# Performance work log

Measured on AMD Instinct MI355X. Metric: run time of the kernel, lower is better.

Reference implementation:

```python
import jax, jax.numpy as jnp
import numpy as np

D_MODEL, D_K, D_V, HEADS = 512, 8, 8, 6
EPS = 1e-5


def setup_inputs() -> dict:
    key = jax.random.key(0)
    ks = jax.random.split(key, 16)
    B, S = 16, 1024
    inp = {
        'q_input': jax.random.normal(ks[0], (B, S, D_MODEL), jnp.float32),
        'k_input': jax.random.normal(ks[1], (B, S, D_MODEL), jnp.float32),
        'v_input': jax.random.normal(ks[2], (B, S, D_MODEL), jnp.float32),
        'mask': jax.random.randint(ks[3], (B, S, S), 0, 2).astype(bool),
        'Wq': jax.random.normal(ks[4], (D_MODEL, D_K * HEADS), jnp.float32) * 0.04,
        'bq': jax.random.normal(ks[5], (D_K * HEADS,), jnp.float32) * 0.02,
        'Wk': jax.random.normal(ks[6], (D_MODEL, D_K * HEADS), jnp.float32) * 0.04,
        'bk': jax.random.normal(ks[7], (D_K * HEADS,), jnp.float32) * 0.02,
        'Wv': jax.random.normal(ks[8], (D_MODEL, D_V * HEADS), jnp.float32) * 0.04,
        'bv': jax.random.normal(ks[9], (D_V * HEADS,), jnp.float32) * 0.02,
        'Wo': jax.random.normal(ks[10], (HEADS * D_K, D_MODEL), jnp.float32) * 0.1,
        'bo': jax.random.normal(ks[11], (D_MODEL,), jnp.float32) * 0.02,
        'ln_w': 1.0 + jax.random.normal(ks[12], (D_MODEL,), jnp.float32) * 0.02,
        'ln_b': jax.random.normal(ks[13], (D_MODEL,), jnp.float32) * 0.02,
    }
    return inp


def reference(q_input, k_input, v_input, mask, Wq, bq, Wk, bk, Wv, bv, Wo, bo, ln_w, ln_b):
    B, S, _ = q_input.shape
    # projections -> [B, H, S, d]
    q_s = (q_input @ Wq + bq).reshape(B, S, HEADS, D_K).transpose(0, 2, 1, 3)
    k_s = (k_input @ Wk + bk).reshape(B, S, HEADS, D_K).transpose(0, 2, 1, 3)
    v_s = (v_input @ Wv + bv).reshape(B, S, HEADS, D_V).transpose(0, 2, 1, 3)
    # scaled dot-product with masked_fill(mask, 1e-9) as in the original (fills VALUE, not -inf)
    scores = jnp.einsum('bhqd,bhkd->bhqk', q_s, k_s) / np.sqrt(D_K).astype(np.float32)
    scores = jnp.where(mask[:, None, :, :], jnp.float32(1e-9), scores)
    attn = jax.nn.softmax(scores, axis=-1)
    out = jnp.einsum('bhqk,bhkd->bhqd', attn, v_s)  # [B,H,S,d_v]
    out = out.transpose(0, 2, 1, 3).reshape(B, S, HEADS * D_K)
    out = out @ Wo + bo
    x = q_input + out  # residual
    mu = jnp.mean(x, axis=-1, keepdims=True)
    var = jnp.var(x, axis=-1, keepdims=True)
    return (x - mu) * jax.lax.rsqrt(var + EPS) * ln_w + ln_b
```

## Files before the change

### kernel.cpp

```cpp
#include <hip/hip_runtime.h>

constexpr int B = 16;
constexpr int S = 1024;
constexpr int DM = 512;
constexpr int H = 6;
constexpr int DK = 8;
constexpr int NJ = H * DK;
constexpr int BS = B * S;
constexpr int WB_ELEMS = 16 * NJ * 32;

typedef __attribute__((ext_vector_type(8))) short bf16x8;
typedef __attribute__((ext_vector_type(8))) _Float16 half8;
typedef __attribute__((ext_vector_type(4))) _Float16 half4;
typedef __attribute__((ext_vector_type(4))) float floatx4;

#define LOG2E 1.4426950408889634f
#define QSCALE (0.35355339059327373f * LOG2E)

__device__ inline ushort f2bf(float f) {
  unsigned int u = __builtin_bit_cast(unsigned int, f);
  return (ushort)((u + 0x7FFFu + ((u >> 16) & 1u)) >> 16);
}

__global__ __launch_bounds__(256) void maskbits_kernel(
    const int* __restrict__ mask, unsigned long long* __restrict__ bits) {
  int wave = threadIdx.x >> 6, lane = threadIdx.x & 63;
  int row = blockIdx.x * 4 + wave;
  const int* mrow = mask + (size_t)row * S;
  unsigned long long* brow = bits + (size_t)row * 16;
  int koff = ((lane >> 5) << 5) + 2 * (lane & 15) + ((lane >> 4) & 1);
#pragma unroll
  for (int c = 0; c < 16; c++) {
    int v = mrow[c * 64 + koff];
    unsigned long long bal = __ballot(v != 0);
    if (lane == 0) brow[c] = bal;
  }
}

__global__ __launch_bounds__(256) void wprep_kernel(
    const float* __restrict__ Wq, const float* __restrict__ Wk,
    const float* __restrict__ Wv, ushort* __restrict__ Wb,
    uint2* __restrict__ VBf) {
  int m = blockIdx.x;
  if (m < 3) {
    const float* W = (m == 0) ? Wq : (m == 1) ? Wk : Wv;
    ushort* dst = Wb + (size_t)m * WB_ELEMS;
    for (int e = threadIdx.x; e < WB_ELEMS; e += 256) {
      int kc = e / 1536;
      int rem = e - kc * 1536;
      int n = rem >> 5, kj = rem & 31;
      dst[e] = f2bf(W[(size_t)(kc * 32 + kj) * NJ + n]);
    }
  } else {
    int bh = m - 3;
    for (int i = threadIdx.x; i < 2048; i += 256) {
      int tile = i >> 5;
      int li = i & 31;
      int g = li >> 3, dd = 8 + (li & 7);
      uint hv = (dd == 8) ? 0x3C003C00u : 0u;
      uint2 val; val.x = hv; val.y = hv;
      VBf[((size_t)bh * 64 + tile) * 64 + g * 16 + dd] = val;
    }
  }
}

__global__ __launch_bounds__(256) void proj_kernel(
    const float* __restrict__ q_in, const float* __restrict__ k_in,
    const float* __restrict__ v_in, const ushort* __restrict__ Wb,
    const float* __restrict__ bq, const float* __restrict__ bk,
    const float* __restrict__ bv,
    ushort* __restrict__ Qo, ushort* __restrict__ Ko, ushort* __restrict__ Vo) {
  int m = blockIdx.y;
  const float* x    = (m == 0) ? q_in : (m == 1) ? k_in : v_in;
  const float* bias = (m == 0) ? bq   : (m == 1) ? bk   : bv;
  ushort* out       = (m == 0) ? Qo   : (m == 1) ? Ko   : Vo;
  float oscale      = (m == 0) ? QSCALE : 1.0f;
  const ushort* Wg  = Wb + (size_t)m * WB_ELEMS;

  __shared__ ushort Wl[WB_ELEMS];

  int t = threadIdx.x;
  {
    const uint4* src = (const uint4*)Wg;
    uint4* dst = (uint4*)Wl;
#pragma unroll
    for (int i = 0; i < 12; i++) dst[t + i * 256] = src[t + i * 256];
  }

  int r0 = blockIdx.x * 64;
  int wave = t >> 6, lane = t & 63;
  int n16 = lane & 15, quad = lane >> 4;
  const float* xrow = x + (size_t)(r0 + wave * 16 + n16) * DM + quad * 8;

  floatx4 acc0 = {0.f, 0.f, 0.f, 0.f};
  floatx4 acc1 = {0.f, 0.f, 0.f, 0.f};
  floatx4 acc2 = {0.f, 0.f, 0.f, 0.f};

  __syncthreads();

#pragma unroll 4
  for (int kc = 0; kc < 16; kc++) {
    float4 xa = *(const float4*)(xrow + kc * 32);
    float4 xb = *(const float4*)(xrow + kc * 32 + 4);
    bf16x8 a;
    a[0] = (short)f2bf(xa.x); a[1] = (short)f2bf(xa.y);
    a[2] = (short)f2bf(xa.z); a[3] = (short)f2bf(xa.w);
    a[4] = (short)f2bf(xb.x); a[5] = (short)f2bf(xb.y);
    a[6] = (short)f2bf(xb.z); a[7] = (short)f2bf(xb.w);
    const ushort* wbase = &Wl[(kc * 48 + n16) * 32 + quad * 8];
    bf16x8 b0 = *(const bf16x8*)(wbase);
    bf16x8 b1 = *(const bf16x8*)(wbase + 16 * 32);
    bf16x8 b2 = *(const bf16x8*)(wbase + 32 * 32);
    acc0 = __builtin_amdgcn_mfma_f32_16x16x32_bf16(a, b0, acc0, 0, 0, 0);
    acc1 = __builtin_amdgcn_mfma_f32_16x16x32_bf16(a, b1, acc1, 0, 0, 0);
    acc2 = __builtin_amdgcn_mfma_f32_16x16x32_bf16(a, b2, acc2, 0, 0, 0);
  }

  int baseR = r0 + wave * 16 + quad * 4;
#pragma unroll
  for (int j = 0; j < 3; j++) {
    floatx4 a = (j == 0) ? acc0 : (j == 1) ? acc1 : acc2;
    int n = j * 16 + n16;
    float bn = bias[n];
    int h = n >> 3, d = n & 7;
#pragma unroll
    for (int r = 0; r < 4; r++) {
      int R = baseR + r;
      int b = R >> 10, s = R & 1023;
      float fv = (a[r] + bn) * oscale;
      if (m == 2) {
        size_t idx =
            ((((size_t)(b * H + h) * 64 + (s >> 4)) * 64) +
             ((s >> 2) & 3) * 16 + d) * 4 + (s & 3);
        out[idx] = __builtin_bit_cast(ushort, (_Float16)fv);
      } else {
        out[(((size_t)(b * H + h)) * S + s) * 8 + d] = f2bf(fv);
      }
    }
  }
}

__global__ __launch_bounds__(256, 6) void attn_kernel(
    const ushort* __restrict__ Qg, const ushort* __restrict__ Kg,
    const ushort* __restrict__ VBg ,
    const uint* __restrict__ bits32, float* __restrict__ A) {
  int bh = blockIdx.x >> 4;
  int qt = blockIdx.x & 15;
  int b = bh / H, h = bh % H;
  int q0 = qt * 64;

  int t = threadIdx.x;
  int wave = t >> 6, lane = t & 63;
  int quad = lane >> 4, n16 = lane & 15;

  const ushort* Kbase = Kg + (size_t)bh * S * 8;
  const uint2* VB = (const uint2*)VBg + (size_t)bh * (64 * 64);

  bf16x8 aq = {0, 0, 0, 0, 0, 0, 0, 0};
  if (quad == 0)
    aq = *(const bf16x8*)&Qg[((size_t)bh * S + q0 + wave * 16 + n16) * 8];

  const uint* mrow = bits32 + (size_t)(b * S + q0 + wave * 16 + n16) * 32;

  floatx4 acc0 = {0.f, 0.f, 0.f, 0.f};
  floatx4 acc1 = {0.f, 0.f, 0.f, 0.f};
  const floatx4 zero = {0.f, 0.f, 0.f, 0.f};
  int sh0 = 2 * quad;

#pragma unroll 1
  for (int cc = 0; cc < 8; cc++) {
    uint4 mq = *(const uint4*)(mrow + cc * 4);
#pragma unroll
    for (int ci = 0; ci < 4; ci++) {
      int c = cc * 4 + ci;
      uint mw = (ci == 0) ? mq.x : (ci == 1) ? mq.y : (ci == 2) ? mq.z : mq.w;

      bf16x8 ak0 = *(const bf16x8*)&Kbase[(size_t)(c * 32 + n16) * 8];
      bf16x8 ak1 = *(const bf16x8*)&Kbase[(size_t)(c * 32 + 16 + n16) * 8];
      uint2 vb0 = VB[(2 * c) * 64 + lane];
      uint2 vb1 = VB[(2 * c + 1) * 64 + lane];

      floatx4 s0 = __builtin_amdgcn_mfma_f32_16x16x32_bf16(ak0, aq, zero, 0, 0, 0);
      floatx4 s1 = __builtin_amdgcn_mfma_f32_16x16x32_bf16(ak1, aq, zero, 0, 0, 0);

      float p0 = exp2f(fminf(s0[0], 15.f)), p1 = exp2f(fminf(s0[1], 15.f));
      float p2 = exp2f(fminf(s0[2], 15.f)), p3 = exp2f(fminf(s0[3], 15.f));
      float p4 = exp2f(fminf(s1[0], 15.f)), p5 = exp2f(fminf(s1[1], 15.f));
      float p6 = exp2f(fminf(s1[2], 15.f)), p7 = exp2f(fminf(s1[3], 15.f));
      uint w0 = __builtin_bit_cast(uint, __builtin_amdgcn_cvt_pkrtz(p0, p1));
      uint w1 = __builtin_bit_cast(uint, __builtin_amdgcn_cvt_pkrtz(p2, p3));
      uint w2 = __builtin_bit_cast(uint, __builtin_amdgcn_cvt_pkrtz(p4, p5));
      uint w3 = __builtin_bit_cast(uint, __builtin_amdgcn_cvt_pkrtz(p6, p7));

      uint m0 = ((mw >> sh0) & 0x10001u) * 0xFFFFu;
      uint m1 = ((mw >> (sh0 + 1)) & 0x10001u) * 0xFFFFu;
      uint m2 = ((mw >> (sh0 + 8)) & 0x10001u) * 0xFFFFu;
      uint m3 = ((mw >> (sh0 + 9)) & 0x10001u) * 0xFFFFu;
      w0 = (m0 & 0x3C003C00u) | (~m0 & w0);
      w1 = (m1 & 0x3C003C00u) | (~m1 & w1);
      w2 = (m2 & 0x3C003C00u) | (~m2 & w2);
      w3 = (m3 & 0x3C003C00u) | (~m3 & w3);

      uint2 pu0; pu0.x = w0; pu0.y = w1;
      uint2 pu1; pu1.x = w2; pu1.y = w3;
      half4 pa0 = __builtin_bit_cast(half4, pu0);
      half4 pa1 = __builtin_bit_cast(half4, pu1);

      acc0 = __builtin_amdgcn_mfma_f32_16x16x16f16(
          pa0, __builtin_bit_cast(half4, vb0), acc0, 0, 0, 0);
      acc1 = __builtin_amdgcn_mfma_f32_16x16x16f16(
          pa1, __builtin_bit_cast(half4, vb1), acc1, 0, 0, 0);
    }
  }

#pragma unroll
  for (int r = 0; r < 4; r++) {
    float sum = acc0[r] + acc1[r];
    float dnm = __shfl(sum, (lane & 48) | 8, 64);
    if (n16 < 8) {
      int qg = q0 + wave * 16 + quad * 4 + r;
      A[((size_t)(b * S + qg)) * NJ + h * 8 + n16] = sum / dnm;
    }
  }
}

__global__ __launch_bounds__(256) void out_ln_kernel(
    const float* __restrict__ A, const float* __restrict__ Wo,
    const float* __restrict__ bo, const float* __restrict__ qin,
    const float* __restrict__ lnw, const float* __restrict__ lnb,
    float* __restrict__ out) {
  int r0 = blockIdx.x * 8;
  int t = threadIdx.x;
  __shared__ float As[8 * NJ];
#pragma unroll
  for (int i = t; i < 8 * NJ; i += 256) As[i] = A[(size_t)r0 * NJ + i];
  __syncthreads();

  int c0 = t, c1 = t + 256;
  float acc0[8], acc1[8];
#pragma unroll
  for (int r = 0; r < 8; r++) { acc0[r] = 0.f; acc1[r] = 0.f; }

#pragma unroll 4
  for (int j = 0; j < NJ; j++) {
    float w0 = Wo[(size_t)j * DM + c0];
    float w1 = Wo[(size_t)j * DM + c1];
#pragma unroll
    for (int r = 0; r < 8; r++) {
      float a = As[r * NJ + j];
      acc0[r] += a * w0;
      acc1[r] += a * w1;
    }
  }

  float b0 = bo[c0], b1 = bo[c1];
  float y0[8], y1[8], ssum[8], sq[8];
#pragma unroll
  for (int r = 0; r < 8; r++) {
    y0[r] = acc0[r] + b0 + qin[(size_t)(r0 + r) * DM + c0];
    y1[r] = acc1[r] + b1 + qin[(size_t)(r0 + r) * DM + c1];
    ssum[r] = y0[r] + y1[r];
    sq[r] = y0[r] * y0[r] + y1[r] * y1[r];
  }

  int wave = t >> 6, lane = t & 63;
  __shared__ float reds[4][8], redq[4][8];
#pragma unroll
  for (int r = 0; r < 8; r++) {
    float s = ssum[r], qq = sq[r];
#pragma unroll
    for (int off = 32; off > 0; off >>= 1) {
      s += __shfl_xor(s, off, 64);
      qq += __shfl_xor(qq, off, 64);
    }
    if (lane == 0) { reds[wave][r] = s; redq[wave][r] = qq; }
  }
  __syncthreads();

  float lw0 = lnw[c0], lw1 = lnw[c1], lb0 = lnb[c0], lb1 = lnb[c1];
#pragma unroll
  for (int r = 0; r < 8; r++) {
    float s = (reds[0][r] + reds[1][r]) + (reds[2][r] + reds[3][r]);
    float qq = (redq[0][r] + redq[1][r]) + (redq[2][r] + redq[3][r]);
    float mu = s * (1.f / 512.f);
    float var = qq * (1.f / 512.f) - mu * mu;
    float rstd = rsqrtf(var + 1e-5f);
    out[(size_t)(r0 + r) * DM + c0] = (y0[r] - mu) * rstd * lw0 + lb0;
    out[(size_t)(r0 + r) * DM + c1] = (y1[r] - mu) * rstd * lw1 + lb1;
  }
}

extern "C" void kernel_launch(void* const* d_in, const int* in_sizes, int n_in,
                              void* d_out, int out_size, void* d_ws,
                              size_t ws_size, hipStream_t stream) {
  const float* q_in = (const float*)d_in[0];
  const float* k_in = (const float*)d_in[1];
  const float* v_in = (const float*)d_in[2];
  const int* mask = (const int*)d_in[3];
  const float* Wq = (const float*)d_in[4];
  const float* bq = (const float*)d_in[5];
  const float* Wk = (const float*)d_in[6];
  const float* bk = (const float*)d_in[7];
  const float* Wv = (const float*)d_in[8];
  const float* bv = (const float*)d_in[9];
  const float* Wo = (const float*)d_in[10];
  const float* bo = (const float*)d_in[11];
  const float* lnw = (const float*)d_in[12];
  const float* lnb = (const float*)d_in[13];
  float* out = (float*)d_out;

  constexpr size_t QKV = (size_t)B * H * S * DK;
  ushort* base = (ushort*)d_ws;
  ushort* Qw = base;
  ushort* Kw = base + QKV;
  ushort* VBw = base + 2 * QKV;
  float* Aw = (float*)(base + 4 * QKV);
  unsigned long long* bits = (unsigned long long*)(Aw + (size_t)BS * NJ);
  ushort* Wb = (ushort*)(bits + (size_t)BS * 16);

  maskbits_kernel<<<BS / 4, 256, 0, stream>>>(mask, bits);
  wprep_kernel<<<3 + B * H, 256, 0, stream>>>(Wq, Wk, Wv, Wb, (uint2*)VBw);
  proj_kernel<<<dim3(BS / 64, 3), 256, 0, stream>>>(
      q_in, k_in, v_in, Wb, bq, bk, bv, Qw, Kw, VBw);
  attn_kernel<<<(B * H * S) / 64, 256, 0, stream>>>(
      Qw, Kw, VBw, (const uint*)bits, Aw);
  out_ln_kernel<<<BS / 8, 256, 0, stream>>>(Aw, Wo, bo, q_in, lnw, lnb, out);
}
```

Before: 305.9 us.

## Prefetch projection inputs, swizzle attention blocks, vectorize output-LN kernel

The projection kernel now issues the first four input-row loads before staging weights into shared memory and keeps a four-deep register prefetch ring in a fully unrolled k loop, so global-load latency overlaps the weight copy and MFMA work. The attention kernel remaps block indices with a swizzle so neighbouring blocks touch different batch-heads, and unrolls the mask-chunk loop by two. The out-projection/LayerNorm kernel gives each thread two adjacent columns accessed as float2, and prefetches the residual input before the shared-memory barrier. Together these add register pressure and change cache access patterns.

```diff
diff --git a/kernel.cpp b/kernel.cpp
--- a/kernel.cpp
+++ b/kernel.cpp
@@ -80,28 +80,39 @@
   __shared__ ushort Wl[WB_ELEMS];
 
   int t = threadIdx.x;
-  {
-    const uint4* src = (const uint4*)Wg;
-    uint4* dst = (uint4*)Wl;
-#pragma unroll
-    for (int i = 0; i < 12; i++) dst[t + i * 256] = src[t + i * 256];
-  }
-
   int r0 = blockIdx.x * 64;
   int wave = t >> 6, lane = t & 63;
   int n16 = lane & 15, quad = lane >> 4;
   const float* xrow = x + (size_t)(r0 + wave * 16 + n16) * DM + quad * 8;
 
+  float4 pa[4], pb[4];
+#pragma unroll
+  for (int i = 0; i < 4; i++) {
+    pa[i] = *(const float4*)(xrow + i * 32);
+    pb[i] = *(const float4*)(xrow + i * 32 + 4);
+  }
+
+  {
+    const uint4* src = (const uint4*)Wg;
+    uint4* dst = (uint4*)Wl;
+#pragma unroll
+    for (int i = 0; i < 12; i++) dst[t + i * 256] = src[t + i * 256];
+  }
+
   floatx4 acc0 = {0.f, 0.f, 0.f, 0.f};
   floatx4 acc1 = {0.f, 0.f, 0.f, 0.f};
   floatx4 acc2 = {0.f, 0.f, 0.f, 0.f};
 
   __syncthreads();
 
-#pragma unroll 4
+#pragma unroll
   for (int kc = 0; kc < 16; kc++) {
-    float4 xa = *(const float4*)(xrow + kc * 32);
-    float4 xb = *(const float4*)(xrow + kc * 32 + 4);
+    float4 xa = pa[kc & 3];
+    float4 xb = pb[kc & 3];
+    if (kc + 4 < 16) {
+      pa[kc & 3] = *(const float4*)(xrow + (kc + 4) * 32);
+      pb[kc & 3] = *(const float4*)(xrow + (kc + 4) * 32 + 4);
+    }
     bf16x8 a;
     a[0] = (short)f2bf(xa.x); a[1] = (short)f2bf(xa.y);
     a[2] = (short)f2bf(xa.z); a[3] = (short)f2bf(xa.w);
@@ -144,8 +155,10 @@
     const ushort* __restrict__ Qg, const ushort* __restrict__ Kg,
     const ushort* __restrict__ VBg ,
     const uint* __restrict__ bits32, float* __restrict__ A) {
-  int bh = blockIdx.x >> 4;
-  int qt = blockIdx.x & 15;
+  int bid = blockIdx.x;
+  int swz = (bid & 7) * 192 + (bid >> 3);
+  int bh = swz >> 4;
+  int qt = swz & 15;
   int b = bh / H, h = bh % H;
   int q0 = qt * 64;
 
@@ -167,7 +180,7 @@
   const floatx4 zero = {0.f, 0.f, 0.f, 0.f};
   int sh0 = 2 * quad;
 
-#pragma unroll 1
+#pragma unroll 2
   for (int cc = 0; cc < 8; cc++) {
     uint4 mq = *(const uint4*)(mrow + cc * 4);
 #pragma unroll
@@ -231,34 +244,39 @@
     float* __restrict__ out) {
   int r0 = blockIdx.x * 8;
   int t = threadIdx.x;
+  int c = t * 2;
+
+  float2 qv[8];
+#pragma unroll
+  for (int r = 0; r < 8; r++)
+    qv[r] = *(const float2*)&qin[(size_t)(r0 + r) * DM + c];
+
   __shared__ float As[8 * NJ];
 #pragma unroll
   for (int i = t; i < 8 * NJ; i += 256) As[i] = A[(size_t)r0 * NJ + i];
   __syncthreads();
 
-  int c0 = t, c1 = t + 256;
-  float acc0[8], acc1[8];
-#pragma unroll
-  for (int r = 0; r < 8; r++) { acc0[r] = 0.f; acc1[r] = 0.f; }
+  float2 acc[8];
+#pragma unroll
+  for (int r = 0; r < 8; r++) { acc[r].x = 0.f; acc[r].y = 0.f; }
 
 #pragma unroll 4
   for (int j = 0; j < NJ; j++) {
-    float w0 = Wo[(size_t)j * DM + c0];
-    float w1 = Wo[(size_t)j * DM + c1];
+    float2 w = *(const float2*)&Wo[(size_t)j * DM + c];
 #pragma unroll
     for (int r = 0; r < 8; r++) {
       float a = As[r * NJ + j];
-      acc0[r] += a * w0;
-      acc1[r] += a * w1;
-    }
-  }
-
-  float b0 = bo[c0], b1 = bo[c1];
+      acc[r].x += a * w.x;
+      acc[r].y += a * w.y;
+    }
+  }
+
+  float2 bv = *(const float2*)&bo[c];
   float y0[8], y1[8], ssum[8], sq[8];
 #pragma unroll
   for (int r = 0; r < 8; r++) {
-    y0[r] = acc0[r] + b0 + qin[(size_t)(r0 + r) * DM + c0];
-    y1[r] = acc1[r] + b1 + qin[(size_t)(r0 + r) * DM + c1];
+    y0[r] = acc[r].x + bv.x + qv[r].x;
+    y1[r] = acc[r].y + bv.y + qv[r].y;
     ssum[r] = y0[r] + y1[r];
     sq[r] = y0[r] * y0[r] + y1[r] * y1[r];
   }
@@ -277,7 +295,8 @@
   }
   __syncthreads();
 
-  float lw0 = lnw[c0], lw1 = lnw[c1], lb0 = lnb[c0], lb1 = lnb[c1];
+  float2 lw = *(const float2*)&lnw[c];
+  float2 lb = *(const float2*)&lnb[c];
 #pragma unroll
   for (int r = 0; r < 8; r++) {
     float s = (reds[0][r] + reds[1][r]) + (reds[2][r] + reds[3][r]);
@@ -285,8 +304,10 @@
     float mu = s * (1.f / 512.f);
     float var = qq * (1.f / 512.f) - mu * mu;
     float rstd = rsqrtf(var + 1e-5f);
-    out[(size_t)(r0 + r) * DM + c0] = (y0[r] - mu) * rstd * lw0 + lb0;
-    out[(size_t)(r0 + r) * DM + c1] = (y1[r] - mu) * rstd * lw1 + lb1;
+    float2 o;
+    o.x = (y0[r] - mu) * rstd * lw.x + lb.x;
+    o.y = (y1[r] - mu) * rstd * lw.y + lb.y;
+    *(float2*)&out[(size_t)(r0 + r) * DM + c] = o;
   }
 }
 
```

Result: slower. 312.1 us (+2.0%).
